# Performance work log

Hardware: AMD Instinct MI355X
Metric: run time of the kernel (lower is better)

Reference implementation:

```python
import jax, jax.numpy as jnp
import numpy as np

N = 20000
E = 640000
D = 128
NORM_FACTOR = 100.0
LN_EPS = 1e-5


def _layer_norm(x, g, b):
    mu = jnp.mean(x, axis=-1, keepdims=True)
    var = jnp.var(x, axis=-1, keepdims=True)
    return (x - mu) * jax.lax.rsqrt(var + LN_EPS) * g + b


def setup_inputs() -> dict:
    key = jax.random.key(0)
    ks = jax.random.split(key, 16)

    def lin(k, fan_in, shape):
        bound = 1.0 / np.sqrt(fan_in)
        return jax.random.uniform(k, shape, jnp.float32, -bound, bound)

    h = jax.random.normal(ks[0], (N, D), jnp.float32)
    distances = jax.random.uniform(ks[1], (E, 1), jnp.float32)
    edges = jax.random.randint(ks[2], (2, E), 0, N, jnp.int64)
    node_mask = jnp.ones((N, 1), jnp.float32)
    edge_mask = jnp.ones((E, 1), jnp.float32)

    return {
        "h": h, "distances": distances, "node_mask": node_mask, "edge_mask": edge_mask,
        # linear: in->out
        "lin_w": lin(ks[3], D, (D, D)), "lin_b": lin(ks[4], D, (D,)),
        # att_mlp: (2D+1)->2D -> 2D->D -> D->1
        "att_w1": lin(ks[5], 2 * D + 1, (2 * D, 2 * D + 1)), "att_b1": lin(ks[5], 2 * D + 1, (2 * D,)),
        "att_w2": lin(ks[6], 2 * D, (D, 2 * D)), "att_b2": lin(ks[6], 2 * D, (D,)),
        "att_w3": lin(ks[7], D, (1, D)), "att_b3": lin(ks[7], D, (1,)),
        # node_mlp: D->D, LN, SiLU, D->D
        "nm_w1": lin(ks[8], D, (D, D)), "nm_b1": lin(ks[8], D, (D,)),
        "nm_ln_g": jnp.ones((D,), jnp.float32), "nm_ln_b": jnp.zeros((D,), jnp.float32),
        "nm_w2": lin(ks[9], D, (D, D)), "nm_b2": lin(ks[9], D, (D,)),
        # final LayerNorm
        "ln_g": jnp.ones((D,), jnp.float32), "ln_b": jnp.zeros((D,), jnp.float32),
        "edges": edges,
    }


def reference(h, distances, node_mask, edge_mask,
              lin_w, lin_b, att_w1, att_b1, att_w2, att_b2, att_w3, att_b3,
              nm_w1, nm_b1, nm_ln_g, nm_ln_b, nm_w2, nm_b2, ln_g, ln_b, edges):
    x = h @ lin_w.T + lin_b                                  # [N, D]
    row, col = edges[0], edges[1]
    x_row = x[row]                                           # [E, D]
    x_col = x[col]                                           # [E, D]

    # DenseAtt
    d = distances * edge_mask
    x_cat = jnp.concatenate([x_row, x_col, d], axis=1)       # [E, 2D+1]
    a = jax.nn.silu(x_cat @ att_w1.T + att_b1)
    a = jax.nn.silu(a @ att_w2.T + att_b2)
    att = jax.nn.sigmoid(a @ att_w3.T + att_b3) * edge_mask  # [E, 1]

    agg = x_col * att                                        # [E, D]
    out = jax.ops.segment_sum(agg, row, num_segments=N) / NORM_FACTOR

    # node_mlp + residual
    o = out @ nm_w1.T + nm_b1
    o = jax.nn.silu(_layer_norm(o, nm_ln_g, nm_ln_b))
    o = o @ nm_w2.T + nm_b2
    hh = o + x

    hh = _layer_norm(hh, ln_g, ln_b)
    hh = jax.nn.silu(hh)                                     # act = SiLU
    return hh
```

## Files before the change

### kernel.cpp

```cpp
#include <hip/hip_runtime.h>
#include <hip/hip_bf16.h>

#define N_NODES 20000
#define E_EDGES 640000
#define DIM 128
#define CAP 96
#define EPB 64
#define NPB 8
#define XST 264

typedef __attribute__((ext_vector_type(8))) short bf16x8;
typedef __attribute__((ext_vector_type(4))) float f32x4;
typedef __attribute__((ext_vector_type(4))) unsigned u32x4;

#define LOG2E 1.44269504f
__device__ __forceinline__ float fsilu(float x) {
    return x * __builtin_amdgcn_rcpf(1.f + __builtin_amdgcn_exp2f(-LOG2E * x));
}
__device__ __forceinline__ float fsig(float x) {
    return __builtin_amdgcn_rcpf(1.f + __builtin_amdgcn_exp2f(-LOG2E * x));
}

__device__ __forceinline__ unsigned short f2bf(float x) {
    union { float f; unsigned u; } v; v.f = x;
    unsigned r = (v.u + 0x7fffu + ((v.u >> 16) & 1u)) >> 16;
    return (unsigned short)r;
}
__device__ __forceinline__ float bf2f(unsigned short s) {
    union { unsigned u; float f; } v; v.u = ((unsigned)s) << 16;
    return v.f;
}
__device__ __forceinline__ unsigned pack_bf16(float lo, float hi) {
    union { float f; unsigned u; } a, b; a.f = lo; b.f = hi;
    unsigned ul = a.u + 0x8000u, uh = b.u + 0x8000u;
    return __builtin_amdgcn_perm(uh, ul, 0x07060302u);
}

#define PRE_PREP_BLOCKS 64
#define PRE_LIN_BLOCKS  625
#define PRE_ADJ_BLOCKS  2500
__global__ __launch_bounds__(256) void pre_kernel(
    const float* __restrict__ w1, const float* __restrict__ w2,
    unsigned short* __restrict__ w1b, float* __restrict__ w1p,
    unsigned short* __restrict__ w2b,
    const float* __restrict__ h, const float* __restrict__ lw,
    const float* __restrict__ lb, float* __restrict__ x,
    unsigned short* __restrict__ xb,
    const int* __restrict__ edges,
    const float* __restrict__ dist, const float* __restrict__ emask,
    int* __restrict__ cnt,
    int* __restrict__ adjc, float2* __restrict__ dm, int E) {
    __shared__ float hs[32][128];
    int b = blockIdx.x;
    int t = threadIdx.x;

    if (b < PRE_PREP_BLOCKS) {
        int i = b * 256 + t;
        const int stride = PRE_PREP_BLOCKS * 256;
        for (int idx = i; idx < 256 * 256; idx += stride) {
            int o = idx >> 8, k = idx & 255;
            w1b[idx] = f2bf(w1[o * 257 + k]);
        }
        for (int idx = i; idx < 128 * 256; idx += stride) {
            int n2 = idx >> 8, p = idx & 255;
            int bb = p & ~31, off = p & 31;
            int ksrc = bb + (off >> 1) + ((off & 1) << 4);
            w2b[idx] = f2bf(w2[n2 * 256 + ksrc]);
        }
        for (int idx = i; idx < 256; idx += stride) {
            int bb = idx & ~31, off = idx & 31;
            int ksrc = bb + (off >> 1) + ((off & 1) << 4);
            w1p[idx] = w1[ksrc * 257 + 256];
        }
    } else if (b < PRE_PREP_BLOCKS + PRE_LIN_BLOCKS) {
        int nb = b - PRE_PREP_BLOCKS;
        int n0 = nb * 32;
        int ch = t & 127, g = t >> 7;
#pragma unroll
        for (int j = 0; j < 16; ++j) hs[g * 16 + j][ch] = h[(size_t)(n0 + g * 16 + j) * DIM + ch];
        __syncthreads();
        float acc[16];
#pragma unroll
        for (int j = 0; j < 16; ++j) acc[j] = 0.f;
        for (int kc = 0; kc < 128; kc += 4) {
            float4 wv = *(const float4*)&lw[(size_t)ch * DIM + kc];
#pragma unroll
            for (int j = 0; j < 16; ++j)
                acc[j] += wv.x * hs[g * 16 + j][kc] + wv.y * hs[g * 16 + j][kc + 1]
                        + wv.z * hs[g * 16 + j][kc + 2] + wv.w * hs[g * 16 + j][kc + 3];
        }
        float bias = lb[ch];
#pragma unroll
        for (int j = 0; j < 16; ++j) {
            float v = acc[j] + bias;
            int n = n0 + g * 16 + j;
            x[(size_t)n * DIM + ch] = v;
            xb[(size_t)n * DIM + ch] = f2bf(v);
        }
    } else {
        int e = (b - PRE_PREP_BLOCKS - PRE_LIN_BLOCKS) * 256 + t;
        if (e < E) {
            int r = edges[e];
            int col = edges[E + e];
            float em = emask[e];
            float dv = dist[e] * em;
            int slot = atomicAdd(&cnt[r], 1);
            if (slot < CAP) {
                adjc[(size_t)r * CAP + slot] = col;
                float2 de; de.x = dv; de.y = em;
                dm[(size_t)r * CAP + slot] = de;
            }
        }
    }
}

__global__ __launch_bounds__(1024) void scan_kernel(const int* __restrict__ cnt,
                                                    int* __restrict__ off) {
    __shared__ int wsum[16], wbase[16];
    int t = threadIdx.x;
    int lane = t & 63, wid = t >> 6;
    int base = t * 20;
    int loc[20];
    int s = 0;
#pragma unroll
    for (int i = 0; i < 20; ++i) {
        int idx = base + i;
        int v = 0;
        if (idx < N_NODES) { v = cnt[idx]; v = v > CAP ? CAP : v; }
        loc[i] = s; s += v;
    }
    int inc = s;
#pragma unroll
    for (int d = 1; d < 64; d <<= 1) {
        int u = __shfl_up(inc, d);
        if (lane >= d) inc += u;
    }
    if (lane == 63) wsum[wid] = inc;
    __syncthreads();
    if (t < 16) {
        int v = wsum[t];
        int inc2 = v;
#pragma unroll
        for (int d = 1; d < 16; d <<= 1) {
            int u = __shfl_up(inc2, d);
            if (t >= d) inc2 += u;
        }
        wbase[t] = inc2 - v;
        if (t == 15) off[N_NODES] = inc2;
    }
    __syncthreads();
    int ex = wbase[wid] + inc - s;
#pragma unroll
    for (int i = 0; i < 20; ++i) {
        int idx = base + i;
        if (idx < N_NODES) off[idx] = ex + loc[i];
    }
}

#define MID_PRC_BLOCKS 1250
#define MID_FLAT_BLOCKS 2500
__global__ __launch_bounds__(256) void mid_kernel(
    const unsigned short* __restrict__ xb,
    const unsigned short* __restrict__ w1b,
    const float* __restrict__ b1,
    unsigned short* __restrict__ prb, unsigned short* __restrict__ pcb,
    const int* __restrict__ adjc, const float2* __restrict__ dm,
    const int* __restrict__ cnt, const int* __restrict__ off,
    int4* __restrict__ flat) {
    int b = blockIdx.x;
    if (b < MID_PRC_BLOCKS) {
        int n0 = b * 16;
        int w = threadIdx.x >> 6, lane = threadIdx.x & 63;
        int lrow = lane & 15, quad = lane >> 4;

        bf16x8 a[4];
#pragma unroll
        for (int kk = 0; kk < 4; ++kk)
            a[kk] = *(const bf16x8*)&xb[(size_t)(n0 + lrow) * DIM + kk * 32 + quad * 8];

        f32x4 z = {0.f, 0.f, 0.f, 0.f};
#pragma unroll
        for (int i = 0; i < 8; ++i) {
            int gt = w * 8 + i;
            int half = gt >> 4;
            int obase = (gt & 15) * 16;
            f32x4 acc = z;
#pragma unroll
            for (int kk = 0; kk < 4; ++kk) {
                bf16x8 bfrag = *(const bf16x8*)&w1b[(size_t)(obase + lrow) * 256 + half * 128 + kk * 32 + quad * 8];
                acc = __builtin_amdgcn_mfma_f32_16x16x32_bf16(a[kk], bfrag, acc, 0, 0, 0);
            }
            int o = obase + lrow;
            if (half == 0) {
                float bias = b1[o];
#pragma unroll
                for (int r = 0; r < 4; ++r)
                    prb[(size_t)(n0 + quad * 4 + r) * 256 + o] = f2bf(acc[r] + bias);
            } else {
#pragma unroll
                for (int r = 0; r < 4; ++r)
                    pcb[(size_t)(n0 + quad * 4 + r) * 256 + o] = f2bf(acc[r]);
            }
        }
    } else {
        int fb = b - MID_PRC_BLOCKS;
        int n0 = fb * NPB;
        int jg = threadIdx.x >> 5, l = threadIdx.x & 31;
        int n = n0 + jg;
        int c = cnt[n]; c = c > CAP ? CAP : c;
        int o = off[n];
        const int* al = adjc + (size_t)n * CAP;
        const float2* dl = dm + (size_t)n * CAP;
        for (int i = l; i < c; i += 32) {
            float2 de = dl[i];
            int4 wv;
            union { float f; int i; } u1, u2; u1.f = de.x; u2.f = de.y;
            wv.x = n; wv.y = al[i]; wv.z = u1.i; wv.w = u2.i;
            flat[o + i] = wv;
        }
    }
}

__global__ __launch_bounds__(512, 4) void edge_kernel(
    const unsigned short* __restrict__ prb, const unsigned short* __restrict__ pcb,
    const int4* __restrict__ flat, const int* __restrict__ off,
    const float* __restrict__ w1p,
    const unsigned short* __restrict__ w2b, const float* __restrict__ b2,
    const float* __restrict__ w3, const float* __restrict__ b3v,
    float* __restrict__ attv) {
    __shared__ unsigned short buf[EPB * XST];
    __shared__ float part[8][EPB];
    __shared__ float w1ps[256];
    __shared__ float dvals[EPB], emv[EPB];
    __shared__ int ridx[EPB], cidx[EPB];

    int tid = threadIdx.x;
    int eb = blockIdx.x * EPB;

    if (tid < EPB) {
        int count = off[N_NODES];
        int idx = eb + tid;
        int4 v;
        if (idx < count) v = flat[idx];
        else { v.x = 0; v.y = 0; v.z = 0; v.w = 0; }
        ridx[tid] = v.x; cidx[tid] = v.y;
        union { int i; float f; } a, bu; a.i = v.z; bu.i = v.w;
        dvals[tid] = a.f; emv[tid] = bu.f;
    }
    if (tid >= 64 && tid < 320) w1ps[tid - 64] = w1p[tid - 64];

    int wave = tid >> 6, lane = tid & 63;
    int lrow = lane & 15, quad = lane >> 4;
    int n2 = wave * 16 + lrow;
    float bias2 = b2[n2];
    float w3v = w3[n2];

    __syncthreads();

    {
        int ge = tid >> 3, cb = tid & 7;
        const unsigned short* prow = prb + (size_t)ridx[ge] * 256 + cb * 32;
        const unsigned short* pcp  = pcb + (size_t)cidx[ge] * 256 + cb * 32;
        float d = dvals[ge];
        const float* wp = &w1ps[cb * 32];
        unsigned u[16];

        bf16x8 pA = *(const bf16x8*)&prow[0];
        bf16x8 pB = *(const bf16x8*)&prow[16];
        bf16x8 qA = *(const bf16x8*)&pcp[0];
        bf16x8 qB = *(const bf16x8*)&pcp[16];
#pragma unroll
        for (int l = 0; l < 8; ++l) {
            float s0 = bf2f((unsigned short)pA[l]) + bf2f((unsigned short)qA[l]) + d * wp[2 * l];
            float s1 = bf2f((unsigned short)pB[l]) + bf2f((unsigned short)qB[l]) + d * wp[2 * l + 1];
            u[l] = pack_bf16(fsilu(s0), fsilu(s1));
        }
        pA = *(const bf16x8*)&prow[8];
        pB = *(const bf16x8*)&prow[24];
        qA = *(const bf16x8*)&pcp[8];
        qB = *(const bf16x8*)&pcp[24];
#pragma unroll
        for (int l = 0; l < 8; ++l) {
            float s0 = bf2f((unsigned short)pA[l]) + bf2f((unsigned short)qA[l]) + d * wp[16 + 2 * l];
            float s1 = bf2f((unsigned short)pB[l]) + bf2f((unsigned short)qB[l]) + d * wp[16 + 2 * l + 1];
            u[8 + l] = pack_bf16(fsilu(s0), fsilu(s1));
        }
        u32x4* w4 = (u32x4*)&buf[ge * XST + cb * 32];
        u32x4 v0 = {u[0], u[1], u[2], u[3]};
        u32x4 v1 = {u[4], u[5], u[6], u[7]};
        u32x4 v2 = {u[8], u[9], u[10], u[11]};
        u32x4 v3 = {u[12], u[13], u[14], u[15]};
        w4[0] = v0; w4[1] = v1; w4[2] = v2; w4[3] = v3;
    }
    __syncthreads();

    f32x4 zz = {0.f, 0.f, 0.f, 0.f};
    f32x4 acc2[4];
#pragma unroll
    for (int mt = 0; mt < 4; ++mt) acc2[mt] = zz;

    for (int kk = 0; kk < 8; ++kk) {
        int ka = kk * 32 + quad * 8;
        bf16x8 bfrag = *(const bf16x8*)&w2b[(size_t)n2 * 256 + ka];
#pragma unroll
        for (int mt = 0; mt < 4; ++mt) {
            bf16x8 a = *(bf16x8*)&buf[(mt * 16 + lrow) * XST + ka];
            acc2[mt] = __builtin_amdgcn_mfma_f32_16x16x32_bf16(a, bfrag, acc2[mt], 0, 0, 0);
        }
    }

    float s[4][4];
#pragma unroll
    for (int mt = 0; mt < 4; ++mt)
#pragma unroll
        for (int r = 0; r < 4; ++r)
            s[mt][r] = fsilu(acc2[mt][r] + bias2) * w3v;
#pragma unroll
    for (int off2 = 1; off2 < 16; off2 <<= 1) {
#pragma unroll
        for (int mt = 0; mt < 4; ++mt)
#pragma unroll
            for (int r = 0; r < 4; ++r)
                s[mt][r] += __shfl_xor(s[mt][r], off2);
    }
    if (lrow == 0) {
#pragma unroll
        for (int mt = 0; mt < 4; ++mt)
#pragma unroll
            for (int r = 0; r < 4; ++r)
                part[wave][mt * 16 + quad * 4 + r] = s[mt][r];
    }
    __syncthreads();

    if (tid < EPB) {
        float ssum = b3v[0];
#pragma unroll
        for (int w = 0; w < 8; ++w) ssum += part[w][tid];
        attv[eb + tid] = fsig(ssum) * emv[tid];
    }
}

__global__ __launch_bounds__(256) void node_kernel(
    const float* __restrict__ attv, const int* __restrict__ adjc,
    const int* __restrict__ cnt, const int* __restrict__ off,
    const unsigned short* __restrict__ xb,
    const float* __restrict__ x,
    const float* __restrict__ w1, const float* __restrict__ bb1,
    const float* __restrict__ lng, const float* __restrict__ lnb,
    const float* __restrict__ w2, const float* __restrict__ bb2,
    const float* __restrict__ gF, const float* __restrict__ bF,
    float* __restrict__ out, int E) {
    __shared__ float atts[NPB][CAP];
    __shared__ int   cols[NPB][CAP];
    __shared__ float outv[NPB][128];
    __shared__ float bufs[NPB][128];
    __shared__ float mu_s[NPB], rs_s[NPB];
    __shared__ int cnts[NPB];

    int t = threadIdx.x;
    int n0 = blockIdx.x * NPB;

    if (t < NPB) { int c = cnt[n0 + t]; cnts[t] = c > CAP ? CAP : c; }
    __syncthreads();

    {
        int jg = t >> 5, l = t & 31;
        int c = cnts[jg];
        const int* al = adjc + (size_t)(n0 + jg) * CAP;
        const float* av = attv + off[n0 + jg];
        for (int i = l; i < c; i += 32) {
            atts[jg][i] = av[i];
            cols[jg][i] = al[i];
        }
    }
    __syncthreads();

    int w = t >> 6, lane = t & 63;
#pragma unroll
    for (int jj = 0; jj < 2; ++jj) {
        int j = w * 2 + jj;
        int c = cnts[j];
        float lo0 = 0.f, hi0 = 0.f, lo1 = 0.f, hi1 = 0.f;
        float lo2 = 0.f, hi2 = 0.f, lo3 = 0.f, hi3 = 0.f;
        int i = 0;
        for (; i + 3 < c; i += 4) {
            unsigned u0 = *(const unsigned*)&xb[(size_t)cols[j][i]     * DIM + lane * 2];
            unsigned u1 = *(const unsigned*)&xb[(size_t)cols[j][i + 1] * DIM + lane * 2];
            unsigned u2 = *(const unsigned*)&xb[(size_t)cols[j][i + 2] * DIM + lane * 2];
            unsigned u3 = *(const unsigned*)&xb[(size_t)cols[j][i + 3] * DIM + lane * 2];
            float w0 = atts[j][i], w1v = atts[j][i + 1], w2v = atts[j][i + 2], w3v = atts[j][i + 3];
            lo0 += w0 * bf2f((unsigned short)(u0 & 0xffff)); hi0 += w0 * bf2f((unsigned short)(u0 >> 16));
            lo1 += w1v * bf2f((unsigned short)(u1 & 0xffff)); hi1 += w1v * bf2f((unsigned short)(u1 >> 16));
            lo2 += w2v * bf2f((unsigned short)(u2 & 0xffff)); hi2 += w2v * bf2f((unsigned short)(u2 >> 16));
            lo3 += w3v * bf2f((unsigned short)(u3 & 0xffff)); hi3 += w3v * bf2f((unsigned short)(u3 >> 16));
        }
        for (; i < c; ++i) {
            unsigned u0 = *(const unsigned*)&xb[(size_t)cols[j][i] * DIM + lane * 2];
            float w0 = atts[j][i];
            lo0 += w0 * bf2f((unsigned short)(u0 & 0xffff));
            hi0 += w0 * bf2f((unsigned short)(u0 >> 16));
        }
        outv[j][lane * 2]     = ((lo0 + lo1) + (lo2 + lo3)) * 0.01f;
        outv[j][lane * 2 + 1] = ((hi0 + hi1) + (hi2 + hi3)) * 0.01f;
    }
    __syncthreads();

    int h = t >> 7, ch = t & 127;
    float xres[4];
#pragma unroll
    for (int jj = 0; jj < 4; ++jj)
        xres[jj] = x[(size_t)(n0 + h * 4 + jj) * DIM + ch];

    float a1[4] = {0, 0, 0, 0};
    for (int kc = 0; kc < 128; kc += 4) {
        float4 wv = *(const float4*)&w1[(size_t)ch * DIM + kc];
#pragma unroll
        for (int jj = 0; jj < 4; ++jj) {
            int j = h * 4 + jj;
            float4 ov = *(const float4*)&outv[j][kc];
            a1[jj] += wv.x * ov.x + wv.y * ov.y + wv.z * ov.z + wv.w * ov.w;
        }
    }
    float bias1 = bb1[ch];
#pragma unroll
    for (int jj = 0; jj < 4; ++jj) bufs[h * 4 + jj][ch] = a1[jj] + bias1;
    __syncthreads();

    {
        int j = t >> 5, l = t & 31;
        float s = 0.f, qq = 0.f;
#pragma unroll
        for (int i = 0; i < 4; ++i) { float v = bufs[j][l + 32 * i]; s += v; qq += v * v; }
#pragma unroll
        for (int off2 = 16; off2; off2 >>= 1) { s += __shfl_xor(s, off2); qq += __shfl_xor(qq, off2); }
        if (l == 0) {
            float mu = s * (1.f / 128.f);
            float var = qq * (1.f / 128.f) - mu * mu;
            mu_s[j] = mu; rs_s[j] = __builtin_amdgcn_rsqf(var + 1e-5f);
        }
    }
    __syncthreads();

    float g = lng[ch], bb = lnb[ch];
    float h2[4];
#pragma unroll
    for (int jj = 0; jj < 4; ++jj) {
        int j = h * 4 + jj;
        h2[jj] = fsilu((bufs[j][ch] - mu_s[j]) * rs_s[j] * g + bb);
    }
    __syncthreads();
#pragma unroll
    for (int jj = 0; jj < 4; ++jj) bufs[h * 4 + jj][ch] = h2[jj];
    __syncthreads();

    float a3[4] = {0, 0, 0, 0};
    for (int kc = 0; kc < 128; kc += 4) {
        float4 wv = *(const float4*)&w2[(size_t)ch * DIM + kc];
#pragma unroll
        for (int jj = 0; jj < 4; ++jj) {
            int j = h * 4 + jj;
            float4 bv = *(const float4*)&bufs[j][kc];
            a3[jj] += wv.x * bv.x + wv.y * bv.y + wv.z * bv.z + wv.w * bv.w;
        }
    }
    float bias2 = bb2[ch];
    float hh[4];
#pragma unroll
    for (int jj = 0; jj < 4; ++jj) hh[jj] = a3[jj] + bias2 + xres[jj];
    __syncthreads();
#pragma unroll
    for (int jj = 0; jj < 4; ++jj) bufs[h * 4 + jj][ch] = hh[jj];
    __syncthreads();

    {
        int j = t >> 5, l = t & 31;
        float s = 0.f, qq = 0.f;
#pragma unroll
        for (int i = 0; i < 4; ++i) { float v = bufs[j][l + 32 * i]; s += v; qq += v * v; }
#pragma unroll
        for (int off2 = 16; off2; off2 >>= 1) { s += __shfl_xor(s, off2); qq += __shfl_xor(qq, off2); }
        if (l == 0) {
            float mu = s * (1.f / 128.f);
            float var = qq * (1.f / 128.f) - mu * mu;
            mu_s[j] = mu; rs_s[j] = __builtin_amdgcn_rsqf(var + 1e-5f);
        }
    }
    __syncthreads();

    float gf = gF[ch], bf = bF[ch];
#pragma unroll
    for (int jj = 0; jj < 4; ++jj) {
        int j = h * 4 + jj;
        float y = (hh[jj] - mu_s[j]) * rs_s[j] * gf + bf;
        out[(size_t)(n0 + j) * DIM + ch] = fsilu(y);
    }
}

extern "C" void kernel_launch(void* const* d_in, const int* in_sizes, int n_in,
                              void* d_out, int out_size, void* d_ws, size_t ws_size,
                              hipStream_t stream) {
    const float* h         = (const float*)d_in[0];
    const float* distances = (const float*)d_in[1];
    const float* edge_mask = (const float*)d_in[3];
    const float* lin_w     = (const float*)d_in[4];
    const float* lin_b     = (const float*)d_in[5];
    const float* att_w1    = (const float*)d_in[6];
    const float* att_b1    = (const float*)d_in[7];
    const float* att_w2    = (const float*)d_in[8];
    const float* att_b2    = (const float*)d_in[9];
    const float* att_w3    = (const float*)d_in[10];
    const float* att_b3    = (const float*)d_in[11];
    const float* nm_w1     = (const float*)d_in[12];
    const float* nm_b1     = (const float*)d_in[13];
    const float* nm_ln_g   = (const float*)d_in[14];
    const float* nm_ln_b   = (const float*)d_in[15];
    const float* nm_w2     = (const float*)d_in[16];
    const float* nm_b2     = (const float*)d_in[17];
    const float* ln_g      = (const float*)d_in[18];
    const float* ln_b      = (const float*)d_in[19];
    const int*   edges     = (const int*)d_in[20];
    float* out = (float*)d_out;

    const int N = N_NODES, E = E_EDGES;

    char* ws = (char*)d_ws;
    float* x            = (float*)ws;            ws += (size_t)N * DIM * 4;
    unsigned short* xb  = (unsigned short*)ws;   ws += (size_t)N * DIM * 2;
    int* cnt            = (int*)ws;              ws += (size_t)N * 4;
    int* off            = (int*)ws;              ws += (size_t)(N + 4) * 4;
    int* adjc           = (int*)ws;              ws += (size_t)N * CAP * 4;
    float2* dm          = (float2*)ws;           ws += (size_t)N * CAP * 8;
    float* attv         = (float*)ws;            ws += (size_t)E * 4;
    unsigned short* w1b = (unsigned short*)ws;   ws += 256 * 256 * 2;
    float* w1p          = (float*)ws;            ws += 256 * 4;
    unsigned short* w2b = (unsigned short*)ws;   ws += 128 * 256 * 2;
    unsigned short* prb = (unsigned short*)ws;   ws += (size_t)N * 256 * 2;
    unsigned short* pcb = (unsigned short*)ws;   ws += (size_t)N * 256 * 2;
    int4* flat          = (int4*)ws;             ws += (size_t)E * 16;

    hipMemsetAsync(cnt, 0, (size_t)N * 4, stream);

    pre_kernel<<<PRE_PREP_BLOCKS + PRE_LIN_BLOCKS + PRE_ADJ_BLOCKS, 256, 0, stream>>>(
        att_w1, att_w2, w1b, w1p, w2b,
        h, lin_w, lin_b, x, xb,
        edges, distances, edge_mask, cnt, adjc, dm, E);
    scan_kernel<<<1, 1024, 0, stream>>>(cnt, off);
    mid_kernel<<<MID_PRC_BLOCKS + MID_FLAT_BLOCKS, 256, 0, stream>>>(
        xb, w1b, att_b1, prb, pcb, adjc, dm, cnt, off, flat);
    edge_kernel<<<E / EPB, 512, 0, stream>>>(prb, pcb, flat, off,
                                             w1p, w2b, att_b2,
                                             att_w3, att_b3, attv);
    node_kernel<<<N / NPB, 256, 0, stream>>>(attv, adjc, cnt, off, xb, x,
                                             nm_w1, nm_b1, nm_ln_g, nm_ln_b,
                                             nm_w2, nm_b2, ln_g, ln_b, out, E);
}
```

Baseline: 413.9 us.

## Vectorize gathers in node and edge kernels and prefetch edge features before sync

The node kernel's neighbor aggregation now has each lane load 16-byte bf16x8 chunks, with four neighbors handled in parallel per wave and combined by cross-lane shuffles, replacing per-lane 4-byte loads. The edge kernel reads its packed edge record directly per thread and issues all gathered feature loads before the first barrier, dropping the shared staging arrays so load latency overlaps the weight staging. The linear prologue reads shared h as float4 instead of scalars. The changes add shuffle reductions and masked tails, and each of eight threads per edge now redundantly loads the same packed record.

```diff
diff --git a/kernel.cpp b/kernel.cpp
--- a/kernel.cpp
+++ b/kernel.cpp
@@ -85,9 +85,10 @@
         for (int kc = 0; kc < 128; kc += 4) {
             float4 wv = *(const float4*)&lw[(size_t)ch * DIM + kc];
 #pragma unroll
-            for (int j = 0; j < 16; ++j)
-                acc[j] += wv.x * hs[g * 16 + j][kc] + wv.y * hs[g * 16 + j][kc + 1]
-                        + wv.z * hs[g * 16 + j][kc + 2] + wv.w * hs[g * 16 + j][kc + 3];
+            for (int j = 0; j < 16; ++j) {
+                float4 hv = *(const float4*)&hs[g * 16 + j][kc];
+                acc[j] += wv.x * hv.x + wv.y * hv.y + wv.z * hv.z + wv.w * hv.w;
+            }
         }
         float bias = lb[ch];
 #pragma unroll
@@ -231,23 +232,31 @@
     __shared__ unsigned short buf[EPB * XST];
     __shared__ float part[8][EPB];
     __shared__ float w1ps[256];
-    __shared__ float dvals[EPB], emv[EPB];
-    __shared__ int ridx[EPB], cidx[EPB];
 
     int tid = threadIdx.x;
     int eb = blockIdx.x * EPB;
-
-    if (tid < EPB) {
-        int count = off[N_NODES];
-        int idx = eb + tid;
-        int4 v;
-        if (idx < count) v = flat[idx];
-        else { v.x = 0; v.y = 0; v.z = 0; v.w = 0; }
-        ridx[tid] = v.x; cidx[tid] = v.y;
-        union { int i; float f; } a, bu; a.i = v.z; bu.i = v.w;
-        dvals[tid] = a.f; emv[tid] = bu.f;
-    }
-    if (tid >= 64 && tid < 320) w1ps[tid - 64] = w1p[tid - 64];
+    int count = off[N_NODES];
+
+    if (tid < 256) w1ps[tid] = w1p[tid];
+
+    int ge = tid >> 3, cb = tid & 7;
+    int eidx = eb + ge;
+    int4 fv;
+    if (eidx < count) fv = flat[eidx];
+    else { fv.x = 0; fv.y = 0; fv.z = 0; fv.w = 0; }
+    const unsigned short* prow = prb + (size_t)fv.x * 256 + cb * 32;
+    const unsigned short* pcp  = pcb + (size_t)fv.y * 256 + cb * 32;
+    union { int i; float f; } ud; ud.i = fv.z;
+    float d = ud.f;
+
+    bf16x8 pA0 = *(const bf16x8*)&prow[0];
+    bf16x8 pB0 = *(const bf16x8*)&prow[16];
+    bf16x8 qA0 = *(const bf16x8*)&pcp[0];
+    bf16x8 qB0 = *(const bf16x8*)&pcp[16];
+    bf16x8 pA1 = *(const bf16x8*)&prow[8];
+    bf16x8 pB1 = *(const bf16x8*)&prow[24];
+    bf16x8 qA1 = *(const bf16x8*)&pcp[8];
+    bf16x8 qB1 = *(const bf16x8*)&pcp[24];
 
     int wave = tid >> 6, lane = tid & 63;
     int lrow = lane & 15, quad = lane >> 4;
@@ -258,31 +267,18 @@
     __syncthreads();
 
     {
-        int ge = tid >> 3, cb = tid & 7;
-        const unsigned short* prow = prb + (size_t)ridx[ge] * 256 + cb * 32;
-        const unsigned short* pcp  = pcb + (size_t)cidx[ge] * 256 + cb * 32;
-        float d = dvals[ge];
         const float* wp = &w1ps[cb * 32];
         unsigned u[16];
-
-        bf16x8 pA = *(const bf16x8*)&prow[0];
-        bf16x8 pB = *(const bf16x8*)&prow[16];
-        bf16x8 qA = *(const bf16x8*)&pcp[0];
-        bf16x8 qB = *(const bf16x8*)&pcp[16];
 #pragma unroll
         for (int l = 0; l < 8; ++l) {
-            float s0 = bf2f((unsigned short)pA[l]) + bf2f((unsigned short)qA[l]) + d * wp[2 * l];
-            float s1 = bf2f((unsigned short)pB[l]) + bf2f((unsigned short)qB[l]) + d * wp[2 * l + 1];
+            float s0 = bf2f((unsigned short)pA0[l]) + bf2f((unsigned short)qA0[l]) + d * wp[2 * l];
+            float s1 = bf2f((unsigned short)pB0[l]) + bf2f((unsigned short)qB0[l]) + d * wp[2 * l + 1];
             u[l] = pack_bf16(fsilu(s0), fsilu(s1));
         }
-        pA = *(const bf16x8*)&prow[8];
-        pB = *(const bf16x8*)&prow[24];
-        qA = *(const bf16x8*)&pcp[8];
-        qB = *(const bf16x8*)&pcp[24];
 #pragma unroll
         for (int l = 0; l < 8; ++l) {
-            float s0 = bf2f((unsigned short)pA[l]) + bf2f((unsigned short)qA[l]) + d * wp[16 + 2 * l];
-            float s1 = bf2f((unsigned short)pB[l]) + bf2f((unsigned short)qB[l]) + d * wp[16 + 2 * l + 1];
+            float s0 = bf2f((unsigned short)pA1[l]) + bf2f((unsigned short)qA1[l]) + d * wp[16 + 2 * l];
+            float s1 = bf2f((unsigned short)pB1[l]) + bf2f((unsigned short)qB1[l]) + d * wp[16 + 2 * l + 1];
             u[8 + l] = pack_bf16(fsilu(s0), fsilu(s1));
         }
         u32x4* w4 = (u32x4*)&buf[ge * XST + cb * 32];
@@ -333,10 +329,14 @@
     __syncthreads();
 
     if (tid < EPB) {
-        float ssum = b3v[0];
-#pragma unroll
-        for (int w = 0; w < 8; ++w) ssum += part[w][tid];
-        attv[eb + tid] = fsig(ssum) * emv[tid];
+        int idx = eb + tid;
+        if (idx < count) {
+            float ssum = b3v[0];
+#pragma unroll
+            for (int w = 0; w < 8; ++w) ssum += part[w][tid];
+            union { int i; float f; } ue; ue.i = flat[idx].w;
+            attv[idx] = fsig(ssum) * ue.f;
+        }
     }
 }
 
@@ -376,32 +376,40 @@
     __syncthreads();
 
     int w = t >> 6, lane = t & 63;
+    int islot = lane >> 4;
+    int co = lane & 15;
 #pragma unroll
     for (int jj = 0; jj < 2; ++jj) {
         int j = w * 2 + jj;
         int c = cnts[j];
-        float lo0 = 0.f, hi0 = 0.f, lo1 = 0.f, hi1 = 0.f;
-        float lo2 = 0.f, hi2 = 0.f, lo3 = 0.f, hi3 = 0.f;
-        int i = 0;
-        for (; i + 3 < c; i += 4) {
-            unsigned u0 = *(const unsigned*)&xb[(size_t)cols[j][i]     * DIM + lane * 2];
-            unsigned u1 = *(const unsigned*)&xb[(size_t)cols[j][i + 1] * DIM + lane * 2];
-            unsigned u2 = *(const unsigned*)&xb[(size_t)cols[j][i + 2] * DIM + lane * 2];
-            unsigned u3 = *(const unsigned*)&xb[(size_t)cols[j][i + 3] * DIM + lane * 2];
-            float w0 = atts[j][i], w1v = atts[j][i + 1], w2v = atts[j][i + 2], w3v = atts[j][i + 3];
-            lo0 += w0 * bf2f((unsigned short)(u0 & 0xffff)); hi0 += w0 * bf2f((unsigned short)(u0 >> 16));
-            lo1 += w1v * bf2f((unsigned short)(u1 & 0xffff)); hi1 += w1v * bf2f((unsigned short)(u1 >> 16));
-            lo2 += w2v * bf2f((unsigned short)(u2 & 0xffff)); hi2 += w2v * bf2f((unsigned short)(u2 >> 16));
-            lo3 += w3v * bf2f((unsigned short)(u3 & 0xffff)); hi3 += w3v * bf2f((unsigned short)(u3 >> 16));
-        }
-        for (; i < c; ++i) {
-            unsigned u0 = *(const unsigned*)&xb[(size_t)cols[j][i] * DIM + lane * 2];
-            float w0 = atts[j][i];
-            lo0 += w0 * bf2f((unsigned short)(u0 & 0xffff));
-            hi0 += w0 * bf2f((unsigned short)(u0 >> 16));
-        }
-        outv[j][lane * 2]     = ((lo0 + lo1) + (lo2 + lo3)) * 0.01f;
-        outv[j][lane * 2 + 1] = ((hi0 + hi1) + (hi2 + hi3)) * 0.01f;
+        float acc[8];
+#pragma unroll
+        for (int k = 0; k < 8; ++k) acc[k] = 0.f;
+        for (int base = 0; base < c; base += 8) {
+            int i0 = base + islot, i1 = base + 4 + islot;
+            bool k0 = i0 < c, k1 = i1 < c;
+            int c0 = cols[j][k0 ? i0 : 0];
+            int c1 = cols[j][k1 ? i1 : 0];
+            float a0 = k0 ? atts[j][i0] : 0.f;
+            float a1 = k1 ? atts[j][i1] : 0.f;
+            bf16x8 q0 = *(const bf16x8*)&xb[(size_t)c0 * DIM + co * 8];
+            bf16x8 q1 = *(const bf16x8*)&xb[(size_t)c1 * DIM + co * 8];
+#pragma unroll
+            for (int k = 0; k < 8; ++k) acc[k] += a0 * bf2f((unsigned short)q0[k]);
+#pragma unroll
+            for (int k = 0; k < 8; ++k) acc[k] += a1 * bf2f((unsigned short)q1[k]);
+        }
+#pragma unroll
+        for (int k = 0; k < 8; ++k) {
+            acc[k] += __shfl_xor(acc[k], 16);
+            acc[k] += __shfl_xor(acc[k], 32);
+        }
+        if (islot == 0) {
+            float4 v0 = {acc[0] * 0.01f, acc[1] * 0.01f, acc[2] * 0.01f, acc[3] * 0.01f};
+            float4 v1 = {acc[4] * 0.01f, acc[5] * 0.01f, acc[6] * 0.01f, acc[7] * 0.01f};
+            *(float4*)&outv[j][co * 8] = v0;
+            *(float4*)&outv[j][co * 8 + 4] = v1;
+        }
     }
     __syncthreads();
 
```

New measurement: 417.9 us. No clear change (+1.0%).
